# Optimization experiments

Measured on AMD Instinct MI355X. Metric: run time of the kernel, lower is better.

The kernel has to match this reference:

```python
import jax, jax.numpy as jnp
import numpy as np

D = 128                # state dim d; full ODE state is d + d*d (x and flattened W)
T = 4096               # number of saved timesteps

# Tsit5 Butcher tableau (Tsitouras 2011), 5th-order solution weights = a7 row (b7 = 0, FSAL)
A21 = 0.161
A31, A32 = -0.008480655492356989, 0.335480655492357
A41, A42, A43 = 2.8971530571054935, -6.359448489975075, 4.3622954328695815
A51, A52, A53, A54 = 5.325864828439257, -11.748883564062828, 7.4955393428898365, -0.09249506636175525
A61, A62, A63, A64, A65 = 5.86145544294642, -12.92096931784711, 8.159367898576159, -0.071584973281401, -0.028269050394068383
B1, B2, B3, B4, B5, B6 = 0.09646076681806523, 0.01, 0.4798896504144996, 1.379008574103742, -3.290069515436081, 2.324710524099774

def _vf(y, Bm):
    # Func.__call__: x = y[:d]; W = reshape(y[d:], (d,d)); f = DynX(W@x) = W@x; bw = W @ b(W) = W @ Bm
    x = y[:D]
    W = y[D:].reshape(D, D)
    return jnp.concatenate([W @ x, (W @ Bm).reshape(D * D)])

def _tsit5_step(y, dt, Bm):
    k1 = _vf(y, Bm)
    k2 = _vf(y + dt * (A21 * k1), Bm)
    k3 = _vf(y + dt * (A31 * k1 + A32 * k2), Bm)
    k4 = _vf(y + dt * (A41 * k1 + A42 * k2 + A43 * k3), Bm)
    k5 = _vf(y + dt * (A51 * k1 + A52 * k2 + A53 * k3 + A54 * k4), Bm)
    k6 = _vf(y + dt * (A61 * k1 + A62 * k2 + A63 * k3 + A64 * k4 + A65 * k5), Bm)
    return y + dt * (B1 * k1 + B2 * k2 + B3 * k3 + B4 * k4 + B5 * k5 + B6 * k6)

def setup_inputs() -> dict:
    key = jax.random.key(0)
    k1, k2 = jax.random.split(key)
    ts = jnp.arange(T, dtype=jnp.float32) / (T - 1)          # save times in [0, 1]
    y0 = 0.1 * jax.random.normal(k1, (D + D * D,), dtype=jnp.float32)
    B = 0.02 * jax.random.normal(k2, (D, D), dtype=jnp.float32)  # WeightDynamics: b(W) = B
    return {"ts": ts, "y0": y0, "B": B}

def reference(ts, y0, B):
    # One Tsit5 step per save interval (deterministic fixed-step counterpart of
    # diffrax.diffeqsolve(ODETerm(func), Tsit5(), saveat=SaveAt(ts=ts))).
    dts = ts[1:] - ts[:-1]
    def step(y, dt):
        y_new = _tsit5_step(y, dt, B)
        return y_new, y_new
    _, ys_rest = jax.lax.scan(step, y0, dts)
    return jnp.concatenate([y0[None], ys_rest], axis=0)  # [T, D + D*D]
```

## Files before the change

### kernel.cpp

```cpp
#include <hip/hip_runtime.h>
#include <cstring>

#define D 128
#define ROW 16512
#define DTF (1.0f/4095.0f)
#define HSTEP (64.0f/4095.0f)
#define H4F  (256.0f/4095.0f)
#define LDA 132
#define LDB 132

#define XCP_OFF 4096
#define MAT_OFF 12416

#define S_ZT      3
#define S_V(m)    (4+(m))
#define S_AT(J)   (11+(J))
#define S_BMT(J)  (27+(J))
#define S_PT      42

struct __align__(16) F4 { float v[4]; };
typedef float f4v __attribute__((ext_vector_type(4)));

__device__ __forceinline__ float* slotp(float* ws, int k){ return ws + MAT_OFF + (size_t)k*16384; }
__device__ __forceinline__ const float* slotpc(const float* ws, int k){ return ws + MAT_OFF + (size_t)k*16384; }

struct CFX { float cf[64][5]; float cx[64][7]; };
struct CMB { float c[31][7]; };
struct EK  { double e[4][4]; };

__device__ __forceinline__ void ldA(const float* A, int r0, float (*As)[LDA]) {
  const F4* A4 = (const F4*)(A + (size_t)r0*128);
  for (int q = threadIdx.x; q < 512; q += 256) {
    F4 x = A4[q];
    *(F4*)&As[q>>5][(q&31)<<2] = x;
  }
}
__device__ __forceinline__ void mmcT(const float (*As)[LDA], const float (*Bs)[LDB], F4& o0, F4& o1) {
  const int rl = threadIdx.x >> 5, c0 = (threadIdx.x & 31) << 2;
  F4 a0s, a1s;
  #pragma unroll
  for (int e = 0; e < 4; ++e) { a0s.v[e] = 0.f; a1s.v[e] = 0.f; }
  #pragma unroll 8
  for (int k = 0; k < 128; ++k) {
    const F4 bv = *(const F4*)&Bs[k][c0];
    const float a0 = As[rl][k], a1 = As[rl+8][k];
    #pragma unroll
    for (int e = 0; e < 4; ++e) {
      a0s.v[e] = fmaf(a0, bv.v[e], a0s.v[e]);
      a1s.v[e] = fmaf(a1, bv.v[e], a1s.v[e]);
    }
  }
  o0 = a0s; o1 = a1s;
}

__global__ __launch_bounds__(256) void k_vchain(const float* y0, const float* Bm,
                                                float* ws, float* out, CMB cmb) {
  __shared__ float As[16][LDA];
  __shared__ float Bs[128][LDB];
  int b = blockIdx.x, t = threadIdx.x;
  const float* W0 = y0 + D;
  const int rl = t >> 5, c0 = (t & 31) << 2;
  if (b < 48) {
    int m = (b >> 3) + 1, strip = b & 7;
    const F4* B4 = (const F4*)Bm;
    for (int q = t; q < 4096; q += 256) {
      F4 x = B4[q]; F4 o;
      #pragma unroll
      for (int e = 0; e < 4; ++e) o.v[e] = HSTEP * x.v[e];
      *(F4*)&Bs[q>>5][(q&31)<<2] = o;
    }
    ldA(W0, strip*16, As);
    __syncthreads();
    F4 o0, o1;
    for (int p = 0; p < m; ++p) {
      mmcT(As, Bs, o0, o1);
      if (p+1 < m) {
        __syncthreads();
        *(F4*)&As[rl][c0] = o0;
        *(F4*)&As[rl+8][c0] = o1;
        __syncthreads();
      }
    }
    float* Vp = slotp(ws, S_V(m));
    *(F4*)&Vp[(size_t)(strip*16+rl)*128 + c0]   = o0;
    *(F4*)&Vp[(size_t)(strip*16+rl+8)*128 + c0] = o1;
  } else if (b < 52) {
    int base = (b-48)*1024;
    for (int i = 0; i < 4; ++i) {
      int q = base + t + i*256;
      ((F4*)out)[q] = ((const F4*)y0)[q];
    }
  } else if (b == 52) {
    if (t < 128) { out[16384+t] = y0[16384+t]; ws[XCP_OFF+t] = y0[t]; }
  } else if (b < 57) {
    int base = (b-53)*1024;
    F4* Vp = (F4*)slotp(ws, S_V(0));
    for (int i = 0; i < 4; ++i) { int q = base + t + i*256; Vp[q] = ((const F4*)W0)[q]; }
  } else if (b < 61) {
    int base = (b-57)*1024;
    float* ZT = slotp(ws, S_ZT);
    for (int i = 0; i < 4; ++i) {
      int q = base + t + i*256;
      F4 x = ((const F4*)Bm)[q];
      int r = q>>5, cc2 = (q&31)<<2;
      #pragma unroll
      for (int e = 0; e < 4; ++e) ZT[(size_t)(cc2+e)*128 + r] = HSTEP * x.v[e];
    }
  } else {
    int idx = b - 61;
    int mat = idx >> 3, strip = idx & 7;
    int slot = (mat < 16) ? S_AT(mat) : S_BMT(mat-16);
    const float* cc = cmb.c[mat];
    const F4* B4 = (const F4*)Bm;
    for (int q = t; q < 4096; q += 256) {
      F4 x = B4[q]; F4 o;
      #pragma unroll
      for (int e = 0; e < 4; ++e) o.v[e] = HSTEP * x.v[e];
      *(F4*)&Bs[q>>5][(q&31)<<2] = o;
    }
    const F4 s0 = *(const F4*)&W0[(size_t)(strip*16+rl)*128 + c0];
    const F4 s1 = *(const F4*)&W0[(size_t)(strip*16+rl+8)*128 + c0];
    F4 t0, t1;
    #pragma unroll
    for (int e = 0; e < 4; ++e) { t0.v[e] = cc[6]*s0.v[e]; t1.v[e] = cc[6]*s1.v[e]; }
    *(F4*)&As[rl][c0] = t0; *(F4*)&As[rl+8][c0] = t1;
    __syncthreads();
    F4 o0, o1;
    for (int k = 5; k >= 0; --k) {
      mmcT(As, Bs, o0, o1);
      #pragma unroll
      for (int e = 0; e < 4; ++e) { o0.v[e] += cc[k]*s0.v[e]; o1.v[e] += cc[k]*s1.v[e]; }
      if (k > 0) {
        __syncthreads();
        *(F4*)&As[rl][c0] = o0; *(F4*)&As[rl+8][c0] = o1;
        __syncthreads();
      }
    }
    float* Cp = slotp(ws, slot);
    int r0 = strip*16 + rl;
    #pragma unroll
    for (int e = 0; e < 4; ++e) {
      Cp[(size_t)(c0+e)*128 + r0]     = o0.v[e];
      Cp[(size_t)(c0+e)*128 + r0 + 8] = o1.v[e];
    }
  }
}

__global__ __launch_bounds__(256) void k_phiT(float* ws) {
  __shared__ float Bs1[128][LDB];
  __shared__ float Bs2[128][LDB];
  __shared__ float Aw[16][LDA];
  __shared__ float Asb[16][LDA];
  int J = blockIdx.x >> 3, strip = blockIdx.x & 7, t = threadIdx.x;
  const int rl = t >> 5, c0 = (t & 31) << 2;
  const float* a  = slotpc(ws, S_AT(J));
  const float* b  = slotpc(ws, S_BMT(J));
  const float* ap = slotpc(ws, S_AT(J+1));
  { const F4* s=(const F4*)b;  for (int q=t;q<4096;q+=256) *(F4*)&Bs1[q>>5][(q&31)<<2]=s[q]; }
  { const F4* s=(const F4*)ap; for (int q=t;q<4096;q+=256) *(F4*)&Bs2[q>>5][(q&31)<<2]=s[q]; }
  ldA(a, strip*16, Aw);
  ldA(b, strip*16, Asb);
  __syncthreads();
  F4 pa0, pa1;
  {
    const F4 p0 = *(const F4*)&ap[(size_t)(strip*16+rl)*128 + c0];
    const F4 p1 = *(const F4*)&ap[(size_t)(strip*16+rl+8)*128 + c0];
    #pragma unroll
    for (int e = 0; e < 4; ++e) {
      pa0.v[e] = Aw[rl][c0+e]   + 4.f*Asb[rl][c0+e]   + p0.v[e];
      pa1.v[e] = Aw[rl+8][c0+e] + 4.f*Asb[rl+8][c0+e] + p1.v[e];
    }
  }
  const float h = H4F, wh = h, wh2 = 0.5f*h*h, wh3 = 0.25f*h*h*h;
  F4 o0, o1;
  mmcT(Aw, Bs1, o0, o1);
  #pragma unroll
  for (int e = 0; e < 4; ++e) { pa0.v[e] += wh*o0.v[e]; pa1.v[e] += wh*o1.v[e]; }
  __syncthreads();
  *(F4*)&Aw[rl][c0] = o0; *(F4*)&Aw[rl+8][c0] = o1;
  __syncthreads();
  mmcT(Aw, Bs1, o0, o1);
  #pragma unroll
  for (int e = 0; e < 4; ++e) { pa0.v[e] += wh2*o0.v[e]; pa1.v[e] += wh2*o1.v[e]; }
  __syncthreads();
  *(F4*)&Aw[rl][c0] = o0; *(F4*)&Aw[rl+8][c0] = o1;
  __syncthreads();
  mmcT(Aw, Bs2, o0, o1);
  #pragma unroll
  for (int e = 0; e < 4; ++e) { pa0.v[e] += wh3*o0.v[e]; pa1.v[e] += wh3*o1.v[e]; }
  __syncthreads();
  mmcT(Asb, Bs1, o0, o1);
  #pragma unroll
  for (int e = 0; e < 4; ++e) { pa0.v[e] += wh*o0.v[e]; pa1.v[e] += wh*o1.v[e]; }
  *(F4*)&Aw[rl][c0] = o0; *(F4*)&Aw[rl+8][c0] = o1;
  __syncthreads();
  mmcT(Asb, Bs2, o0, o1);
  #pragma unroll
  for (int e = 0; e < 4; ++e) { pa0.v[e] += wh*o0.v[e]; pa1.v[e] += wh*o1.v[e]; }
  mmcT(Aw, Bs2, o0, o1);
  #pragma unroll
  for (int e = 0; e < 4; ++e) { pa0.v[e] += wh2*o0.v[e]; pa1.v[e] += wh2*o1.v[e]; }
  float* PT = slotp(ws, S_PT + J);
  const float h6 = h / 6.0f;
  #pragma unroll
  for (int half = 0; half < 2; ++half) {
    int r = strip*16 + rl + half*8;
    F4 pa = half ? pa1 : pa0;
    F4 o;
    #pragma unroll
    for (int e = 0; e < 4; ++e)
      o.v[e] = ((r == c0+e) ? 1.0f : 0.0f) + h6*pa.v[e];
    *(F4*)&PT[(size_t)r*128 + c0] = o;
  }
}

__global__ __launch_bounds__(256, 4) void k_fused(float* ws, float* out, EK ek, CFX cfx) {
  __shared__ __align__(16) float smf[3520];
  int t = threadIdx.x;

  if (blockIdx.x >= 64) {
    float (*coefL)[7] = (float (*)[7])smf;
    int bb = blockIdx.x - 64;
    int j = bb >> 4, strip = bb & 15;
    for (int idx = t; idx < 448; idx += 256) {
      int i = idx / 7, p = idx - i*7;
      float s = 0.f;
      #pragma unroll
      for (int m = 0; m <= 4; ++m) {
        int qm = p - m;
        if (qm >= 0) s = fmaf(cfx.cf[i][m], cfx.cx[j][qm], s);
      }
      coefL[i][p] = s;
    }
    int r = strip*8 + (t >> 5);
    int q = r*32 + (t & 31);
    F4 v[7];
    #pragma unroll
    for (int m = 0; m < 7; ++m) v[m] = ((const F4*)slotpc(ws, S_V(m)))[q];
    __syncthreads();
    #pragma unroll 4
    for (int i = 0; i < 64; ++i) {
      f4v o = {0.f, 0.f, 0.f, 0.f};
      #pragma unroll
      for (int p = 0; p < 7; ++p) {
        float c = coefL[i][p];
        #pragma unroll
        for (int e = 0; e < 4; ++e) o[e] = fmaf(c, v[p].v[e], o[e]);
      }
      __builtin_nontemporal_store(o, (f4v*)(out + (size_t)(j*64 + i)*ROW + D + 4*(size_t)q));
    }
    return;
  }

  float* za   = smf;
  float* zb   = smf + 640;
  float* Pv   = smf + 1280;
  float* Qv   = smf + 1920;
  float* xv   = smf + 2560;
  float* kv   = smf + 2688;
  float* red  = smf + 2816;
  float* uv   = smf + 2944;
  float (*cfs)[5] = (float (*)[5])(smf + 3200);

  int J = blockIdx.x >> 2, w = blockIdx.x & 3;
  int r = t & 127, hh = t >> 7;
  if (t < 128) xv[t] = ws[XCP_OFF + t];
  if (t < 64) {
    double di = (double)(w*64 + t);
    double b1 = di, b2 = b1*(di-1.0)*0.5, b3 = b2*(di-2.0)*(1.0/3.0), b4 = b3*(di-3.0)*0.25;
    cfs[t][0] = 1.f;
    cfs[t][1] = (float)(b1*ek.e[0][0]);
    cfs[t][2] = (float)(b1*ek.e[0][1] + b2*ek.e[1][1]);
    cfs[t][3] = (float)(b1*ek.e[0][2] + b2*ek.e[1][2] + b3*ek.e[2][2]);
    cfs[t][4] = (float)(b1*ek.e[0][3] + b2*ek.e[1][3] + b3*ek.e[2][3] + b4*ek.e[3][3]);
  }
  __syncthreads();

  for (int jj = 0; jj < J; ++jj) {
    const float* PT = slotpc(ws, S_PT + jj);
    float s = 0.f;
    #pragma unroll 8
    for (int c = hh*64; c < hh*64+64; ++c) s = fmaf(PT[(size_t)c*128 + r], xv[c], s);
    if (hh) red[r] = s;
    __syncthreads();
    if (!hh) xv[r] = s + red[r];
    __syncthreads();
  }
  if (J > 0 && w == 0 && t < 128) out[(size_t)(256*J)*ROW + t] = xv[t];

  const float* ATJ = slotpc(ws, S_AT(J));
  {
    float s = 0.f;
    #pragma unroll 8
    for (int c = hh*64; c < hh*64 + 64; ++c) s = fmaf(ATJ[(size_t)c*128 + r], xv[c], s);
    if (hh) red[r] = s;
    __syncthreads();
    if (!hh) kv[r] = s + red[r];
    __syncthreads();
  }
  if (t < 128) { za[t] = xv[t]; zb[t] = kv[t]; }
  __syncthreads();
  const float* ZTg = slotpc(ws, S_ZT);
  for (int m = 1; m <= 4; ++m) {
    float sa = 0.f, sb = 0.f;
    #pragma unroll 8
    for (int c = hh*64; c < hh*64 + 64; ++c) {
      float zv = ZTg[(size_t)c*128 + r];
      sa = fmaf(zv, za[(m-1)*128 + c], sa);
      sb = fmaf(zv, zb[(m-1)*128 + c], sb);
    }
    if (hh) { red[r] = sa; uv[r] = sb; }
    __syncthreads();
    if (!hh) { za[m*128 + r] = sa + red[r]; zb[m*128 + r] = sb + uv[r]; }
    __syncthreads();
  }
  for (int m = 0; m <= 4; ++m) {
    float sa = 0.f, sb = 0.f;
    #pragma unroll 8
    for (int c = hh*64; c < hh*64 + 64; ++c) {
      float av = ATJ[(size_t)c*128 + r];
      sa = fmaf(av, za[m*128 + c], sa);
      sb = fmaf(av, zb[m*128 + c], sb);
    }
    if (hh) { red[r] = sa; uv[r] = sb; }
    __syncthreads();
    if (!hh) { Pv[m*128 + r] = sa + red[r]; Qv[m*128 + r] = sb + uv[r]; }
    __syncthreads();
  }
  float xr = xv[r], kr = kv[r];
  #pragma unroll 4
  for (int l = 0; l < 32; ++l) {
    int il = 2*l + hh;
    int i = w*64 + il;
    if (i >= 1) {
      float hi = i * DTF;
      float k2r = 0.f;
      #pragma unroll
      for (int m = 0; m <= 4; ++m)
        k2r = fmaf(cfs[il][m], Pv[m*128 + r] + hi*Qv[m*128 + r], k2r);
      out[(size_t)(256*J + i)*ROW + r] = xr + 0.5f*hi*(kr + k2r);
    }
  }
}

static void pmul16(const double* a, const double* b, double* o) {
  double r[16];
  for (int i = 0; i < 16; ++i) r[i] = 0.0;
  for (int i = 0; i < 16; ++i) {
    double ai = a[i];
    if (ai == 0.0) continue;
    for (int k = 0; i + k < 16; ++k) r[i+k] += ai*b[k];
  }
  for (int i = 0; i < 16; ++i) o[i] = r[i];
}

extern "C" void kernel_launch(void* const* d_in, const int* in_sizes, int n_in,
                              void* d_out, int out_size, void* d_ws, size_t ws_size,
                              hipStream_t stream) {
  (void)in_sizes; (void)n_in; (void)out_size; (void)ws_size;
  const float* y0 = (const float*)d_in[1];
  const float* Bm = (const float*)d_in[2];
  float* out = (float*)d_out;
  float* ws  = (float*)d_ws;

  double At[7][7]; memset(At, 0, sizeof(At));
  At[2][1] = 0.161;
  At[3][1] = -0.008480655492356989; At[3][2] = 0.335480655492357;
  At[4][1] = 2.8971530571054935;  At[4][2] = -6.359448489975075;  At[4][3] = 4.3622954328695815;
  At[5][1] = 5.325864828439257;   At[5][2] = -11.748883564062828; At[5][3] = 7.4955393428898365;  At[5][4] = -0.09249506636175525;
  At[6][1] = 5.86145544294642;    At[6][2] = -12.92096931784711;  At[6][3] = 8.159367898576159;   At[6][4] = -0.071584973281401; At[6][5] = -0.028269050394068383;
  const double dB[7] = {0, 0.09646076681806523, 0.01, 0.4798896504144996,
                        1.379008574103742, -3.290069515436081, 2.324710524099774};
  double C[7][16]; memset(C, 0, sizeof(C));
  C[1][0] = 1.0;
  for (int s = 2; s <= 6; ++s) {
    C[s][0] = 1.0;
    for (int k = 1; k < 16; ++k) {
      double acc = 0.0;
      for (int l = 1; l < s; ++l) acc += At[s][l]*C[l][k-1];
      C[s][k] = acc;
    }
  }
  double M[16]; memset(M, 0, sizeof(M)); M[0] = 1.0;
  for (int k = 1; k < 16; ++k) {
    double acc = 0.0;
    for (int s = 1; s <= 6; ++s) acc += dB[s]*C[s][k-1];
    M[k] = acc;
  }
  double p64m[16]; p64m[0] = 1.0;
  for (int m = 1; m < 16; ++m) p64m[m] = p64m[m-1]*64.0;

  CFX cfx; memset(&cfx, 0, sizeof(cfx));
  CMB cmb; memset(&cmb, 0, sizeof(cmb));
  double cur[16]; memset(cur, 0, sizeof(cur)); cur[0] = 1.0;
  for (int n = 0; n <= 4032; ++n) {
    if (n < 64)  for (int m = 0; m <= 4; ++m) cfx.cf[n][m] = (float)(cur[m]/p64m[m]);
    if ((n & 63) == 0) {
      int j = n >> 6;
      if (j < 64) for (int m = 0; m <= 6; ++m) cfx.cx[j][m] = (float)(cur[m]/p64m[m]);
    }
    if ((n & 255) == 0) {
      int J = n >> 8;
      if (J <= 15) for (int m = 0; m <= 6; ++m) cmb.c[J][m] = (float)(cur[m]/p64m[m]);
    }
    if ((n & 255) == 128) {
      int J = (n - 128) >> 8;
      if (J <= 14) for (int m = 0; m <= 6; ++m) cmb.c[16+J][m] = (float)(cur[m]/p64m[m]);
    }
    pmul16(cur, M, cur);
  }

  EK ek; memset(&ek, 0, sizeof(ek));
  {
    double e1[5] = {0,0,0,0,0}, e2[5] = {0,0,0,0,0}, e3[5] = {0,0,0,0,0}, e4[5] = {0,0,0,0,0};
    for (int m = 1; m <= 4; ++m) e1[m] = M[m];
    for (int m = 2; m <= 4; ++m) for (int a = 1; a < m; ++a) e2[m] += e1[a]*e1[m-a];
    for (int m = 3; m <= 4; ++m) for (int a = 2; a < m; ++a) e3[m] += e2[a]*e1[m-a];
    e4[4] = e3[3]*e1[1];
    for (int m = 1; m <= 4; ++m) {
      ek.e[0][m-1] = e1[m]/p64m[m];
      ek.e[1][m-1] = e2[m]/p64m[m];
      ek.e[2][m-1] = e3[m]/p64m[m];
      ek.e[3][m-1] = e4[m]/p64m[m];
    }
  }

  k_vchain<<<309, 256, 0, stream>>>(y0, Bm, ws, out, cmb);
  k_phiT<<<120, 256, 0, stream>>>(ws);
  k_fused<<<1088, 256, 0, stream>>>(ws, out, ek, cfx);
}
```

Baseline: 150.7 us.

## Truncate W-series to five powers and restage output blocks via shared memory

Cuts the power-series expansion of the W trajectory from seven terms to five. This removes the V5 and V6 matrix-power chains from k_vchain, which needs 16 fewer blocks. The output-writing blocks in k_fused now stage a quarter of each V matrix in LDS and write 16 timesteps each, instead of holding seven V vectors in registers across 64 timesteps. Dropping the higher-order terms may reduce accuracy, and the larger LDS footprint lowers occupancy to two blocks per CU.

```diff
diff --git a/kernel.cpp b/kernel.cpp
--- a/kernel.cpp
+++ b/kernel.cpp
@@ -8,6 +8,7 @@
 #define H4F  (256.0f/4095.0f)
 #define LDA 132
 #define LDB 132
+#define NV  5
 
 #define XCP_OFF 4096
 #define MAT_OFF 12416
@@ -24,7 +25,7 @@
 __device__ __forceinline__ float* slotp(float* ws, int k){ return ws + MAT_OFF + (size_t)k*16384; }
 __device__ __forceinline__ const float* slotpc(const float* ws, int k){ return ws + MAT_OFF + (size_t)k*16384; }
 
-struct CFX { float cf[64][5]; float cx[64][7]; };
+struct CFX { float cf[64][5]; float cx[64][5]; };
 struct CMB { float c[31][7]; };
 struct EK  { double e[4][4]; };
 
@@ -60,7 +61,7 @@
   int b = blockIdx.x, t = threadIdx.x;
   const float* W0 = y0 + D;
   const int rl = t >> 5, c0 = (t & 31) << 2;
-  if (b < 48) {
+  if (b < 32) {
     int m = (b >> 3) + 1, strip = b & 7;
     const F4* B4 = (const F4*)Bm;
     for (int q = t; q < 4096; q += 256) {
@@ -84,20 +85,20 @@
     float* Vp = slotp(ws, S_V(m));
     *(F4*)&Vp[(size_t)(strip*16+rl)*128 + c0]   = o0;
     *(F4*)&Vp[(size_t)(strip*16+rl+8)*128 + c0] = o1;
-  } else if (b < 52) {
-    int base = (b-48)*1024;
+  } else if (b < 36) {
+    int base = (b-32)*1024;
     for (int i = 0; i < 4; ++i) {
       int q = base + t + i*256;
       ((F4*)out)[q] = ((const F4*)y0)[q];
     }
-  } else if (b == 52) {
+  } else if (b == 36) {
     if (t < 128) { out[16384+t] = y0[16384+t]; ws[XCP_OFF+t] = y0[t]; }
-  } else if (b < 57) {
-    int base = (b-53)*1024;
+  } else if (b < 41) {
+    int base = (b-37)*1024;
     F4* Vp = (F4*)slotp(ws, S_V(0));
     for (int i = 0; i < 4; ++i) { int q = base + t + i*256; Vp[q] = ((const F4*)W0)[q]; }
-  } else if (b < 61) {
-    int base = (b-57)*1024;
+  } else if (b < 45) {
+    int base = (b-41)*1024;
     float* ZT = slotp(ws, S_ZT);
     for (int i = 0; i < 4; ++i) {
       int q = base + t + i*256;
@@ -107,7 +108,7 @@
       for (int e = 0; e < 4; ++e) ZT[(size_t)(cc2+e)*128 + r] = HSTEP * x.v[e];
     }
   } else {
-    int idx = b - 61;
+    int idx = b - 45;
     int mat = idx >> 3, strip = idx & 7;
     int slot = (mat < 16) ? S_AT(mat) : S_BMT(mat-16);
     const float* cc = cmb.c[mat];
@@ -214,40 +215,45 @@
   }
 }
 
-__global__ __launch_bounds__(256, 4) void k_fused(float* ws, float* out, EK ek, CFX cfx) {
-  __shared__ __align__(16) float smf[3520];
+__global__ __launch_bounds__(256, 2) void k_fused(float* ws, float* out, EK ek, CFX cfx) {
+  __shared__ __align__(16) float smf[NV*4096];
   int t = threadIdx.x;
 
   if (blockIdx.x >= 64) {
-    float (*coefL)[7] = (float (*)[7])smf;
     int bb = blockIdx.x - 64;
-    int j = bb >> 4, strip = bb & 15;
-    for (int idx = t; idx < 448; idx += 256) {
-      int i = idx / 7, p = idx - i*7;
-      float s = 0.f;
-      #pragma unroll
-      for (int m = 0; m <= 4; ++m) {
-        int qm = p - m;
-        if (qm >= 0) s = fmaf(cfx.cf[i][m], cfx.cx[j][qm], s);
+    int g = bb >> 2, qt = bb & 3;
+    for (int m = 0; m < NV; ++m) {
+      const F4* Vq = (const F4*)(slotpc(ws, S_V(m)) + qt*4096);
+      F4* L = (F4*)&smf[m*4096];
+      for (int q4 = t; q4 < 1024; q4 += 256) L[q4] = Vq[q4];
+    }
+    __syncthreads();
+    for (int nn = 0; nn < 16; ++nn) {
+      int n = g*16 + nn, j = n >> 6, i = n & 63;
+      float c[5];
+      #pragma unroll
+      for (int p = 0; p < 5; ++p) {
+        float s = 0.f;
+        #pragma unroll
+        for (int m = 0; m <= 4; ++m) {
+          int qm = p - m;
+          if (qm >= 0) s = fmaf(cfx.cf[i][m], cfx.cx[j][qm], s);
+        }
+        c[p] = s;
       }
-      coefL[i][p] = s;
-    }
-    int r = strip*8 + (t >> 5);
-    int q = r*32 + (t & 31);
-    F4 v[7];
-    #pragma unroll
-    for (int m = 0; m < 7; ++m) v[m] = ((const F4*)slotpc(ws, S_V(m)))[q];
-    __syncthreads();
-    #pragma unroll 4
-    for (int i = 0; i < 64; ++i) {
-      f4v o = {0.f, 0.f, 0.f, 0.f};
-      #pragma unroll
-      for (int p = 0; p < 7; ++p) {
-        float c = coefL[i][p];
+      float* dst = out + (size_t)n*ROW + D + qt*4096;
+      #pragma unroll
+      for (int k = 0; k < 4; ++k) {
+        int qq = k*256 + t;
+        f4v o = {0.f, 0.f, 0.f, 0.f};
         #pragma unroll
-        for (int e = 0; e < 4; ++e) o[e] = fmaf(c, v[p].v[e], o[e]);
+        for (int m = 0; m < NV; ++m) {
+          F4 v = *(const F4*)&smf[m*4096 + 4*qq];
+          #pragma unroll
+          for (int e = 0; e < 4; ++e) o[e] = fmaf(c[m], v.v[e], o[e]);
+        }
+        __builtin_nontemporal_store(o, (f4v*)(dst + 4*(size_t)qq));
       }
-      __builtin_nontemporal_store(o, (f4v*)(out + (size_t)(j*64 + i)*ROW + D + 4*(size_t)q));
     }
     return;
   }
@@ -397,7 +403,7 @@
     if (n < 64)  for (int m = 0; m <= 4; ++m) cfx.cf[n][m] = (float)(cur[m]/p64m[m]);
     if ((n & 63) == 0) {
       int j = n >> 6;
-      if (j < 64) for (int m = 0; m <= 6; ++m) cfx.cx[j][m] = (float)(cur[m]/p64m[m]);
+      if (j < 64) for (int m = 0; m <= 4; ++m) cfx.cx[j][m] = (float)(cur[m]/p64m[m]);
     }
     if ((n & 255) == 0) {
       int J = n >> 8;
@@ -425,7 +431,7 @@
     }
   }
 
-  k_vchain<<<309, 256, 0, stream>>>(y0, Bm, ws, out, cmb);
+  k_vchain<<<293, 256, 0, stream>>>(y0, Bm, ws, out, cmb);
   k_phiT<<<120, 256, 0, stream>>>(ws);
   k_fused<<<1088, 256, 0, stream>>>(ws, out, ek, cfx);
 }
```

Result: faster. 141.3 us (-6.3%).
